# Kernel optimization log

Measured on AMD Instinct MI355X. Metric: run time of the kernel, lower is better.

The kernel has to match this reference:

```python
import jax, jax.numpy as jnp
import numpy as np

EMBED = 1024
HEADS = 16
HEAD_DIM = EMBED // HEADS


def setup_inputs() -> dict:
    key = jax.random.key(0)
    ks = jax.random.split(key, 7)
    B, S = 4, 2048
    q = jax.random.normal(ks[0], (B, S, EMBED), dtype=jnp.float32)
    k = jax.random.normal(ks[1], (B, S, EMBED), dtype=jnp.float32)
    v = jax.random.normal(ks[2], (B, S, EMBED), dtype=jnp.float32)
    # causal mask, broadcast over heads: [B, 1, S, S]
    mask = jnp.broadcast_to(jnp.tril(jnp.ones((S, S), dtype=jnp.int32))[None, None], (B, 1, S, S))
    scale = 1.0 / np.sqrt(EMBED)
    w_q = jax.random.normal(ks[3], (EMBED, EMBED), dtype=jnp.float32) * scale
    w_k = jax.random.normal(ks[4], (EMBED, EMBED), dtype=jnp.float32) * scale
    w_v = jax.random.normal(ks[5], (EMBED, EMBED), dtype=jnp.float32) * scale
    w_o = jax.random.normal(ks[6], (EMBED, EMBED), dtype=jnp.float32) * scale
    return {"q": q, "k": k, "v": v, "mask": mask,
            "w_q": w_q, "w_k": w_k, "w_v": w_v, "w_o": w_o}


def reference(q, k, v, mask, w_q, w_k, w_v, w_o):
    B, S, _ = q.shape
    # Linear projections (torch Linear: x @ W^T), split into heads: [B,H,S,D]
    def proj(x, w):
        return (x @ w.T).reshape(B, -1, HEADS, HEAD_DIM).transpose(0, 2, 1, 3)
    qh, kh, vh = proj(q, w_q), proj(k, w_k), proj(v, w_v)
    scores = jnp.einsum('bhqd,bhkd->bhqk', qh, kh) / jnp.sqrt(jnp.float32(HEAD_DIM))
    scores = jnp.where(mask == 0, jnp.float32(-1e9), scores)
    attn = jax.nn.softmax(scores, axis=-1)
    # dropout is identity in eval/reference mode
    x = jnp.einsum('bhqk,bhkd->bhqd', attn, vh)  # [B,H,S,D]
    x = x.transpose(0, 2, 1, 3).reshape(B, S, HEADS * HEAD_DIM)
    return x @ w_o.T
```

## Files before the change

### kernel.cpp

```cpp
#include <hip/hip_runtime.h>

typedef unsigned short u16;
typedef __attribute__((ext_vector_type(8))) short v8s;
typedef __attribute__((ext_vector_type(4))) float v4f;

#define S_LEN  2048
#define NHEADS 16
#define DHEAD  64
#define EMB    1024

#if __has_builtin(__builtin_amdgcn_exp2f)
#define EXP2F __builtin_amdgcn_exp2f
#else
#define EXP2F exp2f
#endif

__device__ __forceinline__ u16 f32_bf16(float f) {
  union { float f; unsigned u; } x; x.f = f;
  unsigned r = x.u + 0x7fffu + ((x.u >> 16) & 1u);
  return (u16)(r >> 16);
}

__device__ __forceinline__ void async16(const void* g, void* l) {
  __builtin_amdgcn_global_load_lds(
      (const __attribute__((address_space(1))) unsigned int*)g,
      (__attribute__((address_space(3))) unsigned int*)l, 16, 0, 0);
}

__global__ __launch_bounds__(256) void cvt_all(
    const float4* __restrict__ s0, const float4* __restrict__ s1,
    const float4* __restrict__ s2, const float4* __restrict__ s3,
    const float4* __restrict__ s4, const float4* __restrict__ s5,
    const float4* __restrict__ s6,
    ushort4* __restrict__ d0, ushort4* __restrict__ d1,
    ushort4* __restrict__ d2, ushort4* __restrict__ d3,
    ushort4* __restrict__ d4, ushort4* __restrict__ d5,
    ushort4* __restrict__ d6, int nbig, int nsmall) {
  const int y = blockIdx.y;
  const float4* s; ushort4* d;
  switch (y) {
    case 0: s = s0; d = d0; break;  case 1: s = s1; d = d1; break;
    case 2: s = s2; d = d2; break;  case 3: s = s3; d = d3; break;
    case 4: s = s4; d = d4; break;  case 5: s = s5; d = d5; break;
    default: s = s6; d = d6; break;
  }
  const int n4 = (y < 3) ? nbig : nsmall;
  for (int i = blockIdx.x * 256 + threadIdx.x; i < n4; i += gridDim.x * 256) {
    const float4 v = s[i];
    ushort4 o;
    o.x = f32_bf16(v.x); o.y = f32_bf16(v.y);
    o.z = f32_bf16(v.z); o.w = f32_bf16(v.w);
    d[i] = o;
  }
}

template <int MODE>
__global__ __launch_bounds__(512, 2) void gemm2ph(
    const u16* __restrict__ A, const u16* __restrict__ W0,
    const u16* __restrict__ W1, const u16* __restrict__ W2,
    u16* __restrict__ Cq, u16* __restrict__ Ck, u16* __restrict__ Cv,
    float* __restrict__ Cf, int mtiles) {
  const int K = 1024;
  const int NKT = 16;
  __shared__ __align__(16) u16 lA[2][128 * 64];
  __shared__ __align__(16) u16 lB[2][128 * 64];
  const int t = threadIdx.x;
  const int lane = t & 63, wv = t >> 6;
  const int wm = wv >> 2, wn = wv & 3;
  const int qr = lane >> 4, cl = lane & 15;

  const int nwg = gridDim.x;
  const int sid = (blockIdx.x & 7) * (nwg >> 3) + (blockIdx.x >> 3);
  const int bm = sid % mtiles, bn = sid / mtiles;
  const int m0 = bm << 7, n0 = bn << 7;
  const int sec = (MODE == 0) ? (m0 >> 13) : 0;
  const u16* W =
      (MODE == 0) ? ((sec == 0) ? W0 : (sec == 1) ? W1 : W2) : W0;

  v4f acc[4][2];
#pragma unroll
  for (int i = 0; i < 4; ++i)
#pragma unroll
    for (int j = 0; j < 2; ++j) acc[i][j] = (v4f){0.f, 0.f, 0.f, 0.f};

  const int srow = t >> 3;
  const int sw = ((t & 7) ^ (srow & 7)) << 3;
  const u16* aS[2];
  const u16* bS[2];
#pragma unroll
  for (int u = 0; u < 2; ++u) {
    aS[u] = A + (size_t)(m0 + srow + u * 64) * K + sw;
    bS[u] = W + (size_t)(n0 + srow + u * 64) * K + sw;
  }

#pragma unroll
  for (int u = 0; u < 2; ++u) async16(aS[u], &lA[0][(t + (u << 9)) << 3]);
#pragma unroll
  for (int u = 0; u < 2; ++u) async16(bS[u], &lB[0][(t + (u << 9)) << 3]);
  __syncthreads();

  for (int kt = 0; kt < NKT; ++kt) {
    const int cur = kt & 1;
    if (kt + 1 < NKT) {
      const int off = (kt + 1) << 6;
#pragma unroll
      for (int u = 0; u < 2; ++u)
        async16(aS[u] + off, &lA[1 - cur][(t + (u << 9)) << 3]);
#pragma unroll
      for (int u = 0; u < 2; ++u)
        async16(bS[u] + off, &lB[1 - cur][(t + (u << 9)) << 3]);
    }
    v8s a[4][2], b[2][2];
#pragma unroll
    for (int mf = 0; mf < 4; ++mf)
#pragma unroll
      for (int kh = 0; kh < 2; ++kh) {
        const int R = wm * 64 + mf * 16 + cl;
        a[mf][kh] =
            *(const v8s*)&lA[cur][R * 64 + ((((kh << 2) + qr) ^ (R & 7)) << 3)];
      }
#pragma unroll
    for (int nf = 0; nf < 2; ++nf)
#pragma unroll
      for (int kh = 0; kh < 2; ++kh) {
        const int R = wn * 32 + nf * 16 + cl;
        b[nf][kh] =
            *(const v8s*)&lB[cur][R * 64 + ((((kh << 2) + qr) ^ (R & 7)) << 3)];
      }
    __builtin_amdgcn_s_setprio(1);
#pragma unroll
    for (int kh = 0; kh < 2; ++kh)
#pragma unroll
      for (int mf = 0; mf < 4; ++mf)
#pragma unroll
        for (int nf = 0; nf < 2; ++nf)
          acc[mf][nf] = __builtin_amdgcn_mfma_f32_16x16x32_bf16(
              a[mf][kh], b[nf][kh], acc[mf][nf], 0, 0, 0);
    __builtin_amdgcn_s_setprio(0);
    __syncthreads();
  }

  if constexpr (MODE == 0) {
    u16* C = (sec == 0) ? Cq : (sec == 1) ? Ck : Cv;
#pragma unroll
    for (int mf = 0; mf < 4; ++mf)
#pragma unroll
      for (int nf = 0; nf < 2; ++nf)
#pragma unroll
        for (int r = 0; r < 4; ++r) {
          const int mloc = (m0 & 8191) + wm * 64 + mf * 16 + qr * 4 + r;
          const int n = n0 + wn * 32 + nf * 16 + cl;
          const int bb = mloc >> 11, s = mloc & (S_LEN - 1);
          const int h = n >> 6, d = n & (DHEAD - 1);
          const size_t idx =
              (sec < 2) ? (((size_t)bb * NHEADS + h) * S_LEN + s) * DHEAD + d
                        : (((size_t)bb * NHEADS + h) * DHEAD + d) * S_LEN + s;
          C[idx] = f32_bf16(acc[mf][nf][r]);
        }
  } else {
#pragma unroll
    for (int mf = 0; mf < 4; ++mf)
#pragma unroll
      for (int nf = 0; nf < 2; ++nf)
#pragma unroll
        for (int r = 0; r < 4; ++r) {
          const int m = m0 + wm * 64 + mf * 16 + qr * 4 + r;
          const int n = n0 + wn * 32 + nf * 16 + cl;
          Cf[(size_t)m * 1024 + n] = acc[mf][nf][r];
        }
  }
}

__global__ __launch_bounds__(256, 2) void attn_causal(
    const u16* __restrict__ Qp, const u16* __restrict__ Kp,
    const u16* __restrict__ VpT, u16* __restrict__ Out) {
  __shared__ __align__(16) u16 lK[2][2][64 * 64];
  __shared__ __align__(16) u16 lV[2][2][64 * 64];
  __shared__ __align__(16) u16 pb[4][32 * 64];
  const int t = threadIdx.x;
  const int lane = t & 63, w = t >> 6;
  const int qr = lane >> 4, cl = lane & 15;
  const int id = blockIdx.x;
  const int col = (id & 7) + ((id >> 6) << 3);
  const int pair = (id >> 3) & 7;
  const int h = col & 15, b = col >> 4;
  const size_t bh = ((size_t)b * NHEADS + h) * S_LEN * DHEAD;
  const u16* Qb = Qp + bh;
  const u16* Kb = Kp + bh;
  const u16* Vb = VpT + bh;

  v8s vone;
#pragma unroll
  for (int j = 0; j < 8; ++j) vone[j] = (short)0x3F80;
  const float SC = 0.125f * 1.4426950408889634f;

#define STAGE_T(TILE, GP, SL)                                                 \
  do {                                                                        \
    const int kn_ = (TILE) << 6;                                              \
    _Pragma("unroll") for (int i_ = 0; i_ < 2; ++i_) {                        \
      const int c_ = t + (i_ << 8);                                           \
      const int krow_ = c_ >> 3, kdc_ = (c_ & 7) ^ (krow_ & 7);               \
      async16(Kb + (size_t)(kn_ + krow_) * DHEAD + kdc_ * 8,                  \
              &lK[GP][SL][(w * 64 + (i_ << 8)) * 8]);                         \
      const int vd_ = c_ >> 3, vkc_ = (c_ & 7) ^ (vd_ & 7);                   \
      async16(Vb + (size_t)vd_ * S_LEN + kn_ + vkc_ * 8,                      \
              &lV[GP][SL][(w * 64 + (i_ << 8)) * 8]);                         \
    }                                                                         \
  } while (0)

  for (int phase = 0; phase < 2; ++phase) {
    const int qt = phase == 0 ? (15 - pair) : pair;
    const int q0 = qt << 7;
    const int wr0 = q0 + w * 32;

    v8s aq[2][2];
#pragma unroll
    for (int mf = 0; mf < 2; ++mf)
#pragma unroll
      for (int kf = 0; kf < 2; ++kf)
        aq[mf][kf] = *(const v8s*)(Qb + (size_t)(wr0 + mf * 16 + cl) * DHEAD +
                                   kf * 32 + qr * 8);

    v4f o[2][4], lac[2];
#pragma unroll
    for (int mf = 0; mf < 2; ++mf) {
      lac[mf] = (v4f){0.f, 0.f, 0.f, 0.f};
#pragma unroll
      for (int nf = 0; nf < 4; ++nf) o[mf][nf] = (v4f){0.f, 0.f, 0.f, 0.f};
    }

    const int ngrp = qt + 1;
    __syncthreads();
    STAGE_T(0, 0, 0);
    STAGE_T(1, 0, 1);

    for (int g = 0; g < ngrp; ++g) {
      const int gp = g & 1;
      __syncthreads();
      if (g + 1 < ngrp) {
        STAGE_T(2 * g + 2, 1 - gp, 0);
        STAGE_T(2 * g + 3, 1 - gp, 1);
      }
#pragma unroll
      for (int sl = 0; sl < 2; ++sl) {
        const int kt = 2 * g + sl;
        const int k0 = kt << 6;
        if (k0 > wr0 + 31) continue;
        const u16* lKc = &lK[gp][sl][0];
        const u16* lVc = &lV[gp][sl][0];

        v4f sacc[2][4];
#pragma unroll
        for (int mf = 0; mf < 2; ++mf)
#pragma unroll
          for (int ni = 0; ni < 4; ++ni) sacc[mf][ni] = (v4f){0.f, 0.f, 0.f, 0.f};
#pragma unroll
        for (int kf = 0; kf < 2; ++kf)
#pragma unroll
          for (int ni = 0; ni < 4; ++ni) {
            const v8s bk = *(const v8s*)&lKc[((ni * 16 + cl) * 8 +
                                             (((kf << 2) + qr) ^ (cl & 7))) * 8];
            sacc[0][ni] = __builtin_amdgcn_mfma_f32_16x16x32_bf16(
                aq[0][kf], bk, sacc[0][ni], 0, 0, 0);
            sacc[1][ni] = __builtin_amdgcn_mfma_f32_16x16x32_bf16(
                aq[1][kf], bk, sacc[1][ni], 0, 0, 0);
          }

#pragma unroll
        for (int mf = 0; mf < 2; ++mf) {
          const int rowb0 = wr0 + mf * 16;
          if (k0 + 63 <= rowb0) {
#pragma unroll
            for (int ni = 0; ni < 4; ++ni) {
              const int kc = ni * 2 + (cl >> 3);
#pragma unroll
              for (int r = 0; r < 4; ++r) {
                const float e = EXP2F(sacc[mf][ni][r] * SC);
                pb[w][((kc * 32 + mf * 16 + r * 4 + qr) << 3) + (cl & 7)] =
                    (u16)(__float_as_uint(e) >> 16);
              }
            }
          } else {
            const int rowb = rowb0 + qr * 4;
#pragma unroll
            for (int ni = 0; ni < 4; ++ni) {
              const int colk = k0 + ni * 16 + cl;
              const int kc = ni * 2 + (cl >> 3);
#pragma unroll
              for (int r = 0; r < 4; ++r) {
                float e = EXP2F(sacc[mf][ni][r] * SC);
                if (colk > rowb + r) e = 0.f;
                pb[w][((kc * 32 + mf * 16 + r * 4 + qr) << 3) + (cl & 7)] =
                    (u16)(__float_as_uint(e) >> 16);
              }
            }
          }
        }

#pragma unroll
        for (int kf = 0; kf < 2; ++kf) {
          const int kc = (kf << 2) + qr;
          const int sig0 = ((cl & 3) << 2) + (cl >> 2);
          const v8s ap0 = *(const v8s*)&pb[w][((kc * 32 + sig0) << 3)];
          const v8s ap1 = *(const v8s*)&pb[w][((kc * 32 + 16 + sig0) << 3)];
          lac[0] = __builtin_amdgcn_mfma_f32_16x16x32_bf16(ap0, vone, lac[0], 0, 0, 0);
          lac[1] = __builtin_amdgcn_mfma_f32_16x16x32_bf16(ap1, vone, lac[1], 0, 0, 0);
#pragma unroll
          for (int nf = 0; nf < 4; ++nf) {
            const v8s bv = *(const v8s*)&lVc[((nf * 16 + cl) * 8 +
                                             (kc ^ (cl & 7))) * 8];
            o[0][nf] = __builtin_amdgcn_mfma_f32_16x16x32_bf16(ap0, bv, o[0][nf], 0, 0, 0);
            o[1][nf] = __builtin_amdgcn_mfma_f32_16x16x32_bf16(ap1, bv, o[1][nf], 0, 0, 0);
          }
        }
      }
    }

#pragma unroll
    for (int mf = 0; mf < 2; ++mf) {
      float inv[4];
#pragma unroll
      for (int r = 0; r < 4; ++r) inv[r] = 1.0f / lac[mf][r];
#pragma unroll
      for (int nf = 0; nf < 4; ++nf)
#pragma unroll
        for (int r = 0; r < 4; ++r) {
          const int row = wr0 + mf * 16 + qr * 4 + r;
          const int colo = h * DHEAD + nf * 16 + cl;
          Out[((size_t)b * S_LEN + row) * EMB + colo] = f32_bf16(o[mf][nf][r] * inv[r]);
        }
    }
  }
#undef STAGE_T
}

extern "C" void kernel_launch(void* const* d_in, const int* in_sizes, int n_in,
                              void* d_out, int out_size, void* d_ws, size_t ws_size,
                              hipStream_t stream) {
  (void)in_sizes; (void)n_in; (void)out_size; (void)ws_size;
  const float* q  = (const float*)d_in[0];
  const float* k  = (const float*)d_in[1];
  const float* v  = (const float*)d_in[2];
  const float* wq = (const float*)d_in[4];
  const float* wk = (const float*)d_in[5];
  const float* wv = (const float*)d_in[6];
  const float* wo = (const float*)d_in[7];
  float* out = (float*)d_out;

  const size_t MT = (size_t)4 * S_LEN * EMB;
  const size_t WT = (size_t)EMB * EMB;
  u16* p = (u16*)d_ws;
  u16* xq = p; p += MT;
  u16* xk = p; p += MT;
  u16* xv = p; p += MT;
  u16* wqb = p; p += WT;
  u16* wkb = p; p += WT;
  u16* wvb = p; p += WT;
  u16* wob = p; p += WT;
  u16* Qp = p; p += MT;
  u16* Kp = p; p += MT;
  u16* Vp = p; p += MT;
  u16* Ao = xq;

  const dim3 blk(256);
  hipLaunchKernelGGL(cvt_all, dim3(512, 7), blk, 0, stream,
                     (const float4*)q, (const float4*)k, (const float4*)v,
                     (const float4*)wq, (const float4*)wk, (const float4*)wv,
                     (const float4*)wo,
                     (ushort4*)xq, (ushort4*)xk, (ushort4*)xv,
                     (ushort4*)wqb, (ushort4*)wkb, (ushort4*)wvb, (ushort4*)wob,
                     (int)(MT / 4), (int)(WT / 4));
  hipLaunchKernelGGL((gemm2ph<0>), dim3(1536), dim3(512), 0, stream,
                     xq, wqb, wkb, wvb, Qp, Kp, Vp, (float*)nullptr, 192);
  hipLaunchKernelGGL(attn_causal, dim3(512), blk, 0, stream, Qp, Kp, Vp, Ao);
  hipLaunchKernelGGL((gemm2ph<1>), dim3(512), dim3(512), 0, stream,
                     Ao, wob, (const u16*)nullptr, (const u16*)nullptr,
                     (u16*)nullptr, (u16*)nullptr, (u16*)nullptr, out, 64);
}
```

Measured before the change: 340.7 us.

## Use 1024-thread GEMM blocks with smaller per-wave tiles; widen bf16 conversion

The projection and output GEMM blocks grow from 8 to 16 waves. Each wave now computes a 32x32 sub-tile instead of 64x32, and each thread issues one async 16-byte load per operand per k-step. The aim is more latency hiding and fewer registers per wave, but each fragment loaded from shared memory now feeds fewer MFMAs, and the aggressive launch bounds could force register caps or spills. The fp32-to-bf16 conversion kernel also processes 8 elements per thread with a 16-byte store, to cut instruction and store overhead.

```diff
diff --git a/kernel.cpp b/kernel.cpp
--- a/kernel.cpp
+++ b/kernel.cpp
@@ -32,30 +32,33 @@
     const float4* __restrict__ s2, const float4* __restrict__ s3,
     const float4* __restrict__ s4, const float4* __restrict__ s5,
     const float4* __restrict__ s6,
-    ushort4* __restrict__ d0, ushort4* __restrict__ d1,
-    ushort4* __restrict__ d2, ushort4* __restrict__ d3,
-    ushort4* __restrict__ d4, ushort4* __restrict__ d5,
-    ushort4* __restrict__ d6, int nbig, int nsmall) {
+    u16* __restrict__ d0, u16* __restrict__ d1,
+    u16* __restrict__ d2, u16* __restrict__ d3,
+    u16* __restrict__ d4, u16* __restrict__ d5,
+    u16* __restrict__ d6, int nbig, int nsmall) {
   const int y = blockIdx.y;
-  const float4* s; ushort4* d;
+  const float4* s; u16* d;
   switch (y) {
     case 0: s = s0; d = d0; break;  case 1: s = s1; d = d1; break;
     case 2: s = s2; d = d2; break;  case 3: s = s3; d = d3; break;
     case 4: s = s4; d = d4; break;  case 5: s = s5; d = d5; break;
     default: s = s6; d = d6; break;
   }
-  const int n4 = (y < 3) ? nbig : nsmall;
-  for (int i = blockIdx.x * 256 + threadIdx.x; i < n4; i += gridDim.x * 256) {
-    const float4 v = s[i];
-    ushort4 o;
-    o.x = f32_bf16(v.x); o.y = f32_bf16(v.y);
-    o.z = f32_bf16(v.z); o.w = f32_bf16(v.w);
-    d[i] = o;
+  const int n8 = (y < 3) ? nbig : nsmall;
+  for (int i = blockIdx.x * 256 + threadIdx.x; i < n8; i += gridDim.x * 256) {
+    const float4 lo = s[2 * i];
+    const float4 hi = s[2 * i + 1];
+    v8s o;
+    o[0] = (short)f32_bf16(lo.x); o[1] = (short)f32_bf16(lo.y);
+    o[2] = (short)f32_bf16(lo.z); o[3] = (short)f32_bf16(lo.w);
+    o[4] = (short)f32_bf16(hi.x); o[5] = (short)f32_bf16(hi.y);
+    o[6] = (short)f32_bf16(hi.z); o[7] = (short)f32_bf16(hi.w);
+    *(v8s*)(d + (size_t)i * 8) = o;
   }
 }
 
 template <int MODE>
-__global__ __launch_bounds__(512, 2) void gemm2ph(
+__global__ __launch_bounds__(1024, 8) void gemm2ph(
     const u16* __restrict__ A, const u16* __restrict__ W0,
     const u16* __restrict__ W1, const u16* __restrict__ W2,
     u16* __restrict__ Cq, u16* __restrict__ Ck, u16* __restrict__ Cv,
@@ -77,45 +80,34 @@
   const u16* W =
       (MODE == 0) ? ((sec == 0) ? W0 : (sec == 1) ? W1 : W2) : W0;
 
-  v4f acc[4][2];
-#pragma unroll
-  for (int i = 0; i < 4; ++i)
+  v4f acc[2][2];
+#pragma unroll
+  for (int i = 0; i < 2; ++i)
 #pragma unroll
     for (int j = 0; j < 2; ++j) acc[i][j] = (v4f){0.f, 0.f, 0.f, 0.f};
 
   const int srow = t >> 3;
-  const int sw = ((t & 7) ^ (srow & 7)) << 3;
-  const u16* aS[2];
-  const u16* bS[2];
-#pragma unroll
-  for (int u = 0; u < 2; ++u) {
-    aS[u] = A + (size_t)(m0 + srow + u * 64) * K + sw;
-    bS[u] = W + (size_t)(n0 + srow + u * 64) * K + sw;
-  }
-
-#pragma unroll
-  for (int u = 0; u < 2; ++u) async16(aS[u], &lA[0][(t + (u << 9)) << 3]);
-#pragma unroll
-  for (int u = 0; u < 2; ++u) async16(bS[u], &lB[0][(t + (u << 9)) << 3]);
+  const int swe = ((t & 7) ^ (srow & 7)) << 3;
+  const u16* aS = A + (size_t)(m0 + srow) * K + swe;
+  const u16* bS = W + (size_t)(n0 + srow) * K + swe;
+
+  async16(aS, &lA[0][t << 3]);
+  async16(bS, &lB[0][t << 3]);
   __syncthreads();
 
   for (int kt = 0; kt < NKT; ++kt) {
     const int cur = kt & 1;
     if (kt + 1 < NKT) {
       const int off = (kt + 1) << 6;
-#pragma unroll
-      for (int u = 0; u < 2; ++u)
-        async16(aS[u] + off, &lA[1 - cur][(t + (u << 9)) << 3]);
-#pragma unroll
-      for (int u = 0; u < 2; ++u)
-        async16(bS[u] + off, &lB[1 - cur][(t + (u << 9)) << 3]);
+      async16(aS + off, &lA[1 - cur][t << 3]);
+      async16(bS + off, &lB[1 - cur][t << 3]);
     }
-    v8s a[4][2], b[2][2];
-#pragma unroll
-    for (int mf = 0; mf < 4; ++mf)
+    v8s a[2][2], b[2][2];
+#pragma unroll
+    for (int mf = 0; mf < 2; ++mf)
 #pragma unroll
       for (int kh = 0; kh < 2; ++kh) {
-        const int R = wm * 64 + mf * 16 + cl;
+        const int R = wm * 32 + mf * 16 + cl;
         a[mf][kh] =
             *(const v8s*)&lA[cur][R * 64 + ((((kh << 2) + qr) ^ (R & 7)) << 3)];
       }
@@ -131,7 +123,7 @@
 #pragma unroll
     for (int kh = 0; kh < 2; ++kh)
 #pragma unroll
-      for (int mf = 0; mf < 4; ++mf)
+      for (int mf = 0; mf < 2; ++mf)
 #pragma unroll
         for (int nf = 0; nf < 2; ++nf)
           acc[mf][nf] = __builtin_amdgcn_mfma_f32_16x16x32_bf16(
@@ -143,12 +135,12 @@
   if constexpr (MODE == 0) {
     u16* C = (sec == 0) ? Cq : (sec == 1) ? Ck : Cv;
 #pragma unroll
-    for (int mf = 0; mf < 4; ++mf)
+    for (int mf = 0; mf < 2; ++mf)
 #pragma unroll
       for (int nf = 0; nf < 2; ++nf)
 #pragma unroll
         for (int r = 0; r < 4; ++r) {
-          const int mloc = (m0 & 8191) + wm * 64 + mf * 16 + qr * 4 + r;
+          const int mloc = (m0 & 8191) + wm * 32 + mf * 16 + qr * 4 + r;
           const int n = n0 + wn * 32 + nf * 16 + cl;
           const int bb = mloc >> 11, s = mloc & (S_LEN - 1);
           const int h = n >> 6, d = n & (DHEAD - 1);
@@ -159,12 +151,12 @@
         }
   } else {
 #pragma unroll
-    for (int mf = 0; mf < 4; ++mf)
+    for (int mf = 0; mf < 2; ++mf)
 #pragma unroll
       for (int nf = 0; nf < 2; ++nf)
 #pragma unroll
         for (int r = 0; r < 4; ++r) {
-          const int m = m0 + wm * 64 + mf * 16 + qr * 4 + r;
+          const int m = m0 + wm * 32 + mf * 16 + qr * 4 + r;
           const int n = n0 + wn * 32 + nf * 16 + cl;
           Cf[(size_t)m * 1024 + n] = acc[mf][nf][r];
         }
@@ -362,18 +354,17 @@
   u16* Vp = p; p += MT;
   u16* Ao = xq;
 
-  const dim3 blk(256);
-  hipLaunchKernelGGL(cvt_all, dim3(512, 7), blk, 0, stream,
+  hipLaunchKernelGGL(cvt_all, dim3(512, 7), dim3(256), 0, stream,
                      (const float4*)q, (const float4*)k, (const float4*)v,
                      (const float4*)wq, (const float4*)wk, (const float4*)wv,
                      (const float4*)wo,
-                     (ushort4*)xq, (ushort4*)xk, (ushort4*)xv,
-                     (ushort4*)wqb, (ushort4*)wkb, (ushort4*)wvb, (ushort4*)wob,
-                     (int)(MT / 4), (int)(WT / 4));
-  hipLaunchKernelGGL((gemm2ph<0>), dim3(1536), dim3(512), 0, stream,
+                     xq, xk, xv, wqb, wkb, wvb, wob,
+                     (int)(MT / 8), (int)(WT / 8));
+  hipLaunchKernelGGL((gemm2ph<0>), dim3(1536), dim3(1024), 0, stream,
                      xq, wqb, wkb, wvb, Qp, Kp, Vp, (float*)nullptr, 192);
-  hipLaunchKernelGGL(attn_causal, dim3(512), blk, 0, stream, Qp, Kp, Vp, Ao);
-  hipLaunchKernelGGL((gemm2ph<1>), dim3(512), dim3(512), 0, stream,
+  hipLaunchKernelGGL(attn_causal, dim3(512), dim3(256), 0, stream,
+                     Qp, Kp, Vp, Ao);
+  hipLaunchKernelGGL((gemm2ph<1>), dim3(512), dim3(1024), 0, stream,
                      Ao, wob, (const u16*)nullptr, (const u16*)nullptr,
                      (u16*)nullptr, (u16*)nullptr, (u16*)nullptr, out, 64);
 }
```

Result: no change. 342.1 us (+0.4%).
